# Kernel optimization log

Measured on AMD Instinct MI355X. Metric: run time of the kernel, lower is better.

## Reference

```python
import jax, jax.numpy as jnp
import numpy as np

STATE = 256
HYPER = 256
QHID = 64
NAGENTS = 8


def _lin_init(key, fan_in, fan_out):
    # torch nn.Linear default init: U(-1/sqrt(fan_in), 1/sqrt(fan_in))
    kw, kb = jax.random.split(key)
    bound = 1.0 / np.sqrt(fan_in)
    W = jax.random.uniform(kw, (fan_in, fan_out), jnp.float32, -bound, bound)
    b = jax.random.uniform(kb, (fan_out,), jnp.float32, -bound, bound)
    return W, b


def setup_inputs() -> dict:
    key = jax.random.key(0)
    ks = jax.random.split(key, 8)
    q_value_batch = jax.random.normal(ks[0], (128, 512, NAGENTS, 1), jnp.float32)
    state_batch = jax.random.normal(ks[1], (128, 512, 1, STATE), jnp.float32)
    W1a, b1a = _lin_init(ks[2], STATE, HYPER)
    W1b, b1b = _lin_init(ks[3], HYPER, NAGENTS * QHID)
    W2a, b2a = _lin_init(ks[4], STATE, HYPER)
    W2b, b2b = _lin_init(ks[5], HYPER, QHID)
    Wb1, bb1 = _lin_init(ks[6], STATE, QHID)
    kb2a, kb2b = jax.random.split(ks[7])
    Wb2a, bb2a = _lin_init(kb2a, STATE, QHID)
    Wb2b, bb2b = _lin_init(kb2b, QHID, 1)
    return {
        "q_value_batch": q_value_batch, "state_batch": state_batch,
        "W1a": W1a, "b1a": b1a, "W1b": W1b, "b1b": b1b,
        "W2a": W2a, "b2a": b2a, "W2b": W2b, "b2b": b2b,
        "Wb1": Wb1, "bb1": bb1,
        "Wb2a": Wb2a, "bb2a": bb2a, "Wb2b": Wb2b, "bb2b": bb2b,
    }


def reference(q_value_batch, state_batch,
              W1a, b1a, W1b, b1b,
              W2a, b2a, W2b, b2b,
              Wb1, bb1, Wb2a, bb2a, Wb2b, bb2b):
    B = q_value_batch.shape[0]
    # flatten (num_episode, episode_limit) -> N
    q = q_value_batch.reshape(-1, 1, NAGENTS)          # [N, 1, A]
    s = state_batch.reshape(-1, STATE)                 # [N, S]
    # hypernet w1: S -> H -> A*Q, abs
    w1 = jnp.abs(jax.nn.relu(s @ W1a + b1a) @ W1b + b1b)
    w1 = w1.reshape(-1, NAGENTS, QHID)                 # [N, A, Q]
    b1 = (s @ Wb1 + bb1)[:, None, :]                   # [N, 1, Q]
    hidden = jax.nn.elu(jnp.einsum('nxa,naq->nxq', q, w1) + b1)  # [N, 1, Q]
    # hypernet w2: S -> H -> Q, abs
    w2 = jnp.abs(jax.nn.relu(s @ W2a + b2a) @ W2b + b2b)[:, :, None]  # [N, Q, 1]
    b2 = (jax.nn.relu(s @ Wb2a + bb2a) @ Wb2b + bb2b)[:, :, None]     # [N, 1, 1]
    q_total = jnp.einsum('nxq,nqo->nxo', hidden, w2) + b2             # [N, 1, 1]
    return q_total.reshape(B, -1, 1)
```

## Files before the change

kernel.cpp:

```cpp
#include <hip/hip_runtime.h>

typedef __bf16 bf16_t;
typedef bf16_t bf16x8 __attribute__((ext_vector_type(8)));
typedef bf16_t bf16x4 __attribute__((ext_vector_type(4)));
typedef float f32x4 __attribute__((ext_vector_type(4)));
typedef float fv4 __attribute__((ext_vector_type(4)));

#define MFMA __builtin_amdgcn_mfma_f32_16x16x32_bf16
#define SWZ(row, off) ((off) ^ (((row) & 7) << 4))

#define F_W1A   0
#define F_W2A   65536
#define F_W1B   131072
#define F_W2B   262144
#define F_WB1   278528
#define F_WB2A  294912

__device__ __forceinline__ bf16x8 cvt8(fv4 a, fv4 b) {
  bf16x8 v;
  v[0]=(bf16_t)a[0]; v[1]=(bf16_t)a[1]; v[2]=(bf16_t)a[2]; v[3]=(bf16_t)a[3];
  v[4]=(bf16_t)b[0]; v[5]=(bf16_t)b[1]; v[6]=(bf16_t)b[2]; v[7]=(bf16_t)b[3];
  return v;
}

__global__ __launch_bounds__(256) void cvt_frag(
    const float* __restrict__ W1a, const float* __restrict__ W2a,
    const float* __restrict__ W1b, const float* __restrict__ W2b,
    const float* __restrict__ Wb1, const float* __restrict__ Wb2a,
    bf16_t* __restrict__ ws)
{
  int gid = blockIdx.x * 256 + threadIdx.x;
  const float* src; int start, base, nout;
  if (gid < 8192)       { src = W1a;  start = 0;     base = F_W1A;  nout = 256; }
  else if (gid < 16384) { src = W2a;  start = 8192;  base = F_W2A;  nout = 256; }
  else if (gid < 32768) { src = W1b;  start = 16384; base = F_W1B;  nout = 512; }
  else if (gid < 34816) { src = W2b;  start = 32768; base = F_W2B;  nout = 64;  }
  else if (gid < 36864) { src = Wb1;  start = 34816; base = F_WB1;  nout = 64;  }
  else                  { src = Wb2a; start = 36864; base = F_WB2A; nout = 64;  }
  int local = gid - start;
  int t = local >> 9, kk = (local >> 6) & 7, l = local & 63;
  int n  = t * 16 + (l & 15);
  int k0 = kk * 32 + (l >> 4) * 8;
  bf16x8 v;
  #pragma unroll
  for (int j = 0; j < 8; ++j) v[j] = (bf16_t)src[(k0 + j) * nout + n];
  *(bf16x8*)(ws + base + (size_t)local * 8) = v;
}

#define FRAG(base, tile, kk) \
  (*(const bf16x8*)(ws + (base) + ((size_t)(((tile) * 8 + (kk))) << 9) + lane * 8))

__global__ __launch_bounds__(512) void qmix_f4(
    const float* __restrict__ s, const float* __restrict__ q,
    const bf16_t* __restrict__ ws,
    const float* __restrict__ b1a, const float* __restrict__ b2a,
    const float* __restrict__ b1b, const float* __restrict__ b2b,
    const float* __restrict__ bb1, const float* __restrict__ bb2a,
    const float* __restrict__ Wb2b, const float* __restrict__ bb2b,
    float* __restrict__ out)
{
  __shared__ __align__(16) char sT[64 * 512];
  __shared__ __align__(16) char h1T[64 * 512];
  __shared__ __align__(16) char h2T[64 * 512];
  __shared__ __align__(16) char b1T[64 * 128];
  __shared__ __align__(16) char w2T[64 * 128];
  __shared__ __align__(16) char hidT[2][64 * 256];
  __shared__ float b2part[4][64];

  const int tid = threadIdx.x, wave = tid >> 6, lane = tid & 63;
  const int r16 = lane & 15, g = lane >> 4;
  const int row0 = blockIdx.x * 256;
  const int srow = tid >> 3, sc = tid & 7;

  {
    const fv4* p = (const fv4*)(s + (size_t)(row0 + srow) * 256 + sc * 32);
    #pragma unroll
    for (int j = 0; j < 4; ++j) {
      fv4 a = __builtin_nontemporal_load(p + j * 2);
      fv4 b = __builtin_nontemporal_load(p + j * 2 + 1);
      *(bf16x8*)(&sT[srow * 512 + SWZ(srow, sc * 64 + j * 16)]) = cvt8(a, b);
    }
  }
  __syncthreads();

  const float bb2b0 = bb2b[0];
  const int smBase = (wave < 4) ? (F_WB1 + wave * 4096) : (F_WB2A + (wave - 4) * 4096);

  #pragma unroll 1
  for (int rt = 0; rt < 4; ++rt) {
    const int rowt = row0 + rt * 64;
    {
      f32x4 acc[2][4];
      #pragma unroll
      for (int t = 0; t < 2; ++t)
        #pragma unroll
        for (int h = 0; h < 4; ++h) acc[t][h] = (f32x4)0.f;
      #pragma unroll 2
      for (int kk = 0; kk < 8; ++kk) {
        bf16x8 A0 = FRAG(F_W1A, wave, kk);
        bf16x8 A1 = FRAG(F_W1A, wave + 8, kk);
        #pragma unroll
        for (int h = 0; h < 4; ++h) {
          int rr = h * 16 + r16;
          bf16x8 B = *(const bf16x8*)(&sT[rr * 512 + SWZ(rr, kk * 64 + g * 16)]);
          acc[0][h] = MFMA(A0, B, acc[0][h], 0, 0, 0);
          acc[1][h] = MFMA(A1, B, acc[1][h], 0, 0, 0);
        }
      }
      #pragma unroll
      for (int t8 = 0; t8 < 2; ++t8) {
        float4 bh = *(const float4*)(b1a + (wave + t8 * 8) * 16 + 4 * g);
        #pragma unroll
        for (int h = 0; h < 4; ++h) {
          int rr = h * 16 + r16;
          f32x4 x = acc[t8][h];
          bf16x4 v;
          v[0]=(bf16_t)fmaxf(x[0]+bh.x,0.f); v[1]=(bf16_t)fmaxf(x[1]+bh.y,0.f);
          v[2]=(bf16_t)fmaxf(x[2]+bh.z,0.f); v[3]=(bf16_t)fmaxf(x[3]+bh.w,0.f);
          *(bf16x4*)(&h1T[rr * 512 + SWZ(rr, (wave + t8 * 8) * 32 + 8 * g)]) = v;
        }
      }
    }
    {
      f32x4 acc[2][4];
      #pragma unroll
      for (int t = 0; t < 2; ++t)
        #pragma unroll
        for (int h = 0; h < 4; ++h) acc[t][h] = (f32x4)0.f;
      #pragma unroll 2
      for (int kk = 0; kk < 8; ++kk) {
        bf16x8 A0 = FRAG(F_W2A, wave, kk);
        bf16x8 A1 = FRAG(F_W2A, wave + 8, kk);
        #pragma unroll
        for (int h = 0; h < 4; ++h) {
          int rr = h * 16 + r16;
          bf16x8 B = *(const bf16x8*)(&sT[rr * 512 + SWZ(rr, kk * 64 + g * 16)]);
          acc[0][h] = MFMA(A0, B, acc[0][h], 0, 0, 0);
          acc[1][h] = MFMA(A1, B, acc[1][h], 0, 0, 0);
        }
      }
      #pragma unroll
      for (int t8 = 0; t8 < 2; ++t8) {
        float4 bh = *(const float4*)(b2a + (wave + t8 * 8) * 16 + 4 * g);
        #pragma unroll
        for (int h = 0; h < 4; ++h) {
          int rr = h * 16 + r16;
          f32x4 x = acc[t8][h];
          bf16x4 v;
          v[0]=(bf16_t)fmaxf(x[0]+bh.x,0.f); v[1]=(bf16_t)fmaxf(x[1]+bh.y,0.f);
          v[2]=(bf16_t)fmaxf(x[2]+bh.z,0.f); v[3]=(bf16_t)fmaxf(x[3]+bh.w,0.f);
          *(bf16x4*)(&h2T[rr * 512 + SWZ(rr, (wave + t8 * 8) * 32 + 8 * g)]) = v;
        }
      }
    }
    {
      f32x4 aS[4];
      #pragma unroll
      for (int h = 0; h < 4; ++h) aS[h] = (f32x4)0.f;
      #pragma unroll
      for (int kk = 0; kk < 8; ++kk) {
        bf16x8 A = *(const bf16x8*)(ws + smBase + ((size_t)kk << 9) + lane * 8);
        #pragma unroll
        for (int h = 0; h < 4; ++h) {
          int rr = h * 16 + r16;
          bf16x8 B = *(const bf16x8*)(&sT[rr * 512 + SWZ(rr, kk * 64 + g * 16)]);
          aS[h] = MFMA(A, B, aS[h], 0, 0, 0);
        }
      }
      if (wave < 4) {
        float4 bb = *(const float4*)(bb1 + wave * 16 + 4 * g);
        #pragma unroll
        for (int h = 0; h < 4; ++h) {
          int rr = h * 16 + r16;
          bf16x4 o;
          o[0]=(bf16_t)(aS[h][0]+bb.x); o[1]=(bf16_t)(aS[h][1]+bb.y);
          o[2]=(bf16_t)(aS[h][2]+bb.z); o[3]=(bf16_t)(aS[h][3]+bb.w);
          *(bf16x4*)(&b1T[rr * 128 + wave * 32 + 8 * g]) = o;
        }
      } else {
        float4 ba = *(const float4*)(bb2a + (wave - 4) * 16 + 4 * g);
        float4 wv = *(const float4*)(Wb2b + (wave - 4) * 16 + 4 * g);
        #pragma unroll
        for (int h = 0; h < 4; ++h) {
          int rr = h * 16 + r16;
          f32x4 x = aS[h];
          float part = fmaxf(x[0]+ba.x,0.f)*wv.x + fmaxf(x[1]+ba.y,0.f)*wv.y
                     + fmaxf(x[2]+ba.z,0.f)*wv.z + fmaxf(x[3]+ba.w,0.f)*wv.w;
          part += __shfl_xor(part, 16); part += __shfl_xor(part, 32);
          if (lane < 16) b2part[wave - 4][rr] = part;
        }
      }
    }
    __syncthreads();

    fv4 pf[8];
    if (rt < 3) {
      const fv4* p = (const fv4*)(s + (size_t)(rowt + 64 + srow) * 256 + sc * 32);
      #pragma unroll
      for (int j = 0; j < 8; ++j) pf[j] = __builtin_nontemporal_load(p + j);
    }
    {
      const int tq = wave & 3, hs = wave >> 2;
      f32x4 av[2]; av[0] = (f32x4)0.f; av[1] = (f32x4)0.f;
      #pragma unroll
      for (int kk = 0; kk < 8; ++kk) {
        bf16x8 A = FRAG(F_W2B, tq, kk);
        #pragma unroll
        for (int hh = 0; hh < 2; ++hh) {
          int rr = hs * 32 + hh * 16 + r16;
          bf16x8 B = *(const bf16x8*)(&h2T[rr * 512 + SWZ(rr, kk * 64 + g * 16)]);
          av[hh] = MFMA(A, B, av[hh], 0, 0, 0);
        }
      }
      float4 bv = *(const float4*)(b2b + tq * 16 + 4 * g);
      #pragma unroll
      for (int hh = 0; hh < 2; ++hh) {
        int rr = hs * 32 + hh * 16 + r16;
        bf16x4 o;
        o[0]=(bf16_t)fabsf(av[hh][0]+bv.x); o[1]=(bf16_t)fabsf(av[hh][1]+bv.y);
        o[2]=(bf16_t)fabsf(av[hh][2]+bv.z); o[3]=(bf16_t)fabsf(av[hh][3]+bv.w);
        *(bf16x4*)(&w2T[rr * 128 + tq * 32 + 8 * g]) = o;
      }
    }
    {
      const int tq = wave & 3, ah = wave >> 2;
      #pragma unroll 1
      for (int h = 0; h < 4; ++h) {
        const int rr = h * 16 + r16;
        bf16x8 B[8];
        #pragma unroll
        for (int kk = 0; kk < 8; ++kk)
          B[kk] = *(const bf16x8*)(&h1T[rr * 512 + SWZ(rr, kk * 64 + g * 16)]);
        f32x4 hid = (f32x4)0.f;
        #pragma unroll 2
        for (int aa = 0; aa < 4; ++aa) {
          const int a = ah * 4 + aa;
          f32x4 a2 = (f32x4)0.f;
          #pragma unroll
          for (int kk = 0; kk < 8; ++kk) {
            bf16x8 A = FRAG(F_W1B, a * 4 + tq, kk);
            a2 = MFMA(A, B[kk], a2, 0, 0, 0);
          }
          float qa = q[(size_t)(rowt + rr) * 8 + a];
          float4 bb = *(const float4*)(b1b + a * 64 + tq * 16 + 4 * g);
          hid[0] += qa * fabsf(a2[0] + bb.x);
          hid[1] += qa * fabsf(a2[1] + bb.y);
          hid[2] += qa * fabsf(a2[2] + bb.z);
          hid[3] += qa * fabsf(a2[3] + bb.w);
        }
        *(f32x4*)(&hidT[ah][rr * 256 + SWZ(rr, tq * 64 + g * 16)]) = hid;
      }
    }
    if (rt < 3) {
      #pragma unroll
      for (int j = 0; j < 4; ++j)
        *(bf16x8*)(&sT[srow * 512 + SWZ(srow, sc * 64 + j * 16)]) =
            cvt8(pf[j * 2], pf[j * 2 + 1]);
    }
    __syncthreads();
    {
      const int row = tid >> 3, c = tid & 7;
      f32x4 sA0 = *(const f32x4*)(&hidT[0][row * 256 + SWZ(row, c * 32)]);
      f32x4 sA1 = *(const f32x4*)(&hidT[0][row * 256 + SWZ(row, c * 32 + 16)]);
      f32x4 sB0 = *(const f32x4*)(&hidT[1][row * 256 + SWZ(row, c * 32)]);
      f32x4 sB1 = *(const f32x4*)(&hidT[1][row * 256 + SWZ(row, c * 32 + 16)]);
      bf16x8 b1v = *(const bf16x8*)(&b1T[row * 128 + c * 16]);
      bf16x8 wv  = *(const bf16x8*)(&w2T[row * 128 + c * 16]);
      float d = 0.f;
      #pragma unroll
      for (int e = 0; e < 4; ++e) {
        float h0 = sA0[e] + sB0[e] + (float)b1v[e];
        float h1 = sA1[e] + sB1[e] + (float)b1v[4 + e];
        h0 = h0 > 0.f ? h0 : (__expf(h0) - 1.f);
        h1 = h1 > 0.f ? h1 : (__expf(h1) - 1.f);
        d += h0 * (float)wv[e] + h1 * (float)wv[4 + e];
      }
      d += __shfl_xor(d, 1); d += __shfl_xor(d, 2); d += __shfl_xor(d, 4);
      if (c == 0) {
        float b2v = b2part[0][row] + b2part[1][row] + b2part[2][row]
                  + b2part[3][row] + bb2b0;
        out[rowt + row] = d + b2v;
      }
    }
    __syncthreads();
  }
}

extern "C" void kernel_launch(void* const* d_in, const int* in_sizes, int n_in,
                              void* d_out, int out_size, void* d_ws, size_t ws_size,
                              hipStream_t stream) {
  const float* q    = (const float*)d_in[0];
  const float* s    = (const float*)d_in[1];
  const float* W1a  = (const float*)d_in[2];
  const float* b1a  = (const float*)d_in[3];
  const float* W1b  = (const float*)d_in[4];
  const float* b1b  = (const float*)d_in[5];
  const float* W2a  = (const float*)d_in[6];
  const float* b2a  = (const float*)d_in[7];
  const float* W2b  = (const float*)d_in[8];
  const float* b2b  = (const float*)d_in[9];
  const float* Wb1  = (const float*)d_in[10];
  const float* bb1  = (const float*)d_in[11];
  const float* Wb2a = (const float*)d_in[12];
  const float* bb2a = (const float*)d_in[13];
  const float* Wb2b = (const float*)d_in[14];
  const float* bb2b = (const float*)d_in[15];
  bf16_t* ws = (bf16_t*)d_ws;
  float* out = (float*)d_out;

  int N  = in_sizes[0] / 8;
  int nb = N / 256;

  cvt_frag<<<152, 256, 0, stream>>>(W1a, W2a, W1b, W2b, Wb1, Wb2a, ws);
  qmix_f4<<<nb, 512, 0, stream>>>(s, q, ws, b1a, b2a, b1b, b2b,
                                  bb1, bb2a, Wb2b, bb2b, out);
}
```

Before: 122.9 us.

## Fuse state-layer GEMMs into one pass and reuse W1b fragments across rows

Measured after the change: 152.4 us. 24.0% more time.

```diff
diff --git a/kernel.cpp b/kernel.cpp
--- a/kernel.cpp
+++ b/kernel.cpp
@@ -50,7 +50,7 @@
 #define FRAG(base, tile, kk) \
   (*(const bf16x8*)(ws + (base) + ((size_t)(((tile) * 8 + (kk))) << 9) + lane * 8))
 
-__global__ __launch_bounds__(512) void qmix_f4(
+__global__ __launch_bounds__(512) void qmix_f5(
     const float* __restrict__ s, const float* __restrict__ q,
     const bf16_t* __restrict__ ws,
     const float* __restrict__ b1a, const float* __restrict__ b2a,
@@ -64,7 +64,8 @@
   __shared__ __align__(16) char h2T[64 * 512];
   __shared__ __align__(16) char b1T[64 * 128];
   __shared__ __align__(16) char w2T[64 * 128];
-  __shared__ __align__(16) char hidT[2][64 * 256];
+  __shared__ __align__(16) float hidT[2][64 * 68];
+  __shared__ float qT[512];
   __shared__ float b2part[4][64];
 
   const int tid = threadIdx.x, wave = tid >> 6, lane = tid & 63;
@@ -80,6 +81,7 @@
       fv4 b = __builtin_nontemporal_load(p + j * 2 + 1);
       *(bf16x8*)(&sT[srow * 512 + SWZ(srow, sc * 64 + j * 16)]) = cvt8(a, b);
     }
+    qT[tid] = q[(size_t)row0 * 8 + tid];
   }
   __syncthreads();
 
@@ -90,81 +92,44 @@
   for (int rt = 0; rt < 4; ++rt) {
     const int rowt = row0 + rt * 64;
     {
-      f32x4 acc[2][4];
-      #pragma unroll
-      for (int t = 0; t < 2; ++t)
+      f32x4 acc[5][4];
+      #pragma unroll
+      for (int t = 0; t < 5; ++t)
         #pragma unroll
         for (int h = 0; h < 4; ++h) acc[t][h] = (f32x4)0.f;
       #pragma unroll 2
       for (int kk = 0; kk < 8; ++kk) {
         bf16x8 A0 = FRAG(F_W1A, wave, kk);
         bf16x8 A1 = FRAG(F_W1A, wave + 8, kk);
+        bf16x8 A2 = FRAG(F_W2A, wave, kk);
+        bf16x8 A3 = FRAG(F_W2A, wave + 8, kk);
+        bf16x8 A4 = *(const bf16x8*)(ws + smBase + ((size_t)kk << 9) + lane * 8);
         #pragma unroll
         for (int h = 0; h < 4; ++h) {
           int rr = h * 16 + r16;
           bf16x8 B = *(const bf16x8*)(&sT[rr * 512 + SWZ(rr, kk * 64 + g * 16)]);
           acc[0][h] = MFMA(A0, B, acc[0][h], 0, 0, 0);
           acc[1][h] = MFMA(A1, B, acc[1][h], 0, 0, 0);
+          acc[2][h] = MFMA(A2, B, acc[2][h], 0, 0, 0);
+          acc[3][h] = MFMA(A3, B, acc[3][h], 0, 0, 0);
+          acc[4][h] = MFMA(A4, B, acc[4][h], 0, 0, 0);
         }
       }
       #pragma unroll
       for (int t8 = 0; t8 < 2; ++t8) {
-        float4 bh = *(const float4*)(b1a + (wave + t8 * 8) * 16 + 4 * g);
-        #pragma unroll
-        for (int h = 0; h < 4; ++h) {
-          int rr = h * 16 + r16;
-          f32x4 x = acc[t8][h];
-          bf16x4 v;
-          v[0]=(bf16_t)fmaxf(x[0]+bh.x,0.f); v[1]=(bf16_t)fmaxf(x[1]+bh.y,0.f);
-          v[2]=(bf16_t)fmaxf(x[2]+bh.z,0.f); v[3]=(bf16_t)fmaxf(x[3]+bh.w,0.f);
-          *(bf16x4*)(&h1T[rr * 512 + SWZ(rr, (wave + t8 * 8) * 32 + 8 * g)]) = v;
-        }
-      }
-    }
-    {
-      f32x4 acc[2][4];
-      #pragma unroll
-      for (int t = 0; t < 2; ++t)
-        #pragma unroll
-        for (int h = 0; h < 4; ++h) acc[t][h] = (f32x4)0.f;
-      #pragma unroll 2
-      for (int kk = 0; kk < 8; ++kk) {
-        bf16x8 A0 = FRAG(F_W2A, wave, kk);
-        bf16x8 A1 = FRAG(F_W2A, wave + 8, kk);
-        #pragma unroll
-        for (int h = 0; h < 4; ++h) {
-          int rr = h * 16 + r16;
-          bf16x8 B = *(const bf16x8*)(&sT[rr * 512 + SWZ(rr, kk * 64 + g * 16)]);
-          acc[0][h] = MFMA(A0, B, acc[0][h], 0, 0, 0);
-          acc[1][h] = MFMA(A1, B, acc[1][h], 0, 0, 0);
-        }
-      }
-      #pragma unroll
-      for (int t8 = 0; t8 < 2; ++t8) {
-        float4 bh = *(const float4*)(b2a + (wave + t8 * 8) * 16 + 4 * g);
-        #pragma unroll
-        for (int h = 0; h < 4; ++h) {
-          int rr = h * 16 + r16;
-          f32x4 x = acc[t8][h];
-          bf16x4 v;
-          v[0]=(bf16_t)fmaxf(x[0]+bh.x,0.f); v[1]=(bf16_t)fmaxf(x[1]+bh.y,0.f);
-          v[2]=(bf16_t)fmaxf(x[2]+bh.z,0.f); v[3]=(bf16_t)fmaxf(x[3]+bh.w,0.f);
-          *(bf16x4*)(&h2T[rr * 512 + SWZ(rr, (wave + t8 * 8) * 32 + 8 * g)]) = v;
-        }
-      }
-    }
-    {
-      f32x4 aS[4];
-      #pragma unroll
-      for (int h = 0; h < 4; ++h) aS[h] = (f32x4)0.f;
-      #pragma unroll
-      for (int kk = 0; kk < 8; ++kk) {
-        bf16x8 A = *(const bf16x8*)(ws + smBase + ((size_t)kk << 9) + lane * 8);
-        #pragma unroll
-        for (int h = 0; h < 4; ++h) {
-          int rr = h * 16 + r16;
-          bf16x8 B = *(const bf16x8*)(&sT[rr * 512 + SWZ(rr, kk * 64 + g * 16)]);
-          aS[h] = MFMA(A, B, aS[h], 0, 0, 0);
+        float4 bh1 = *(const float4*)(b1a + (wave + t8 * 8) * 16 + 4 * g);
+        float4 bh2 = *(const float4*)(b2a + (wave + t8 * 8) * 16 + 4 * g);
+        #pragma unroll
+        for (int h = 0; h < 4; ++h) {
+          int rr = h * 16 + r16;
+          f32x4 x1 = acc[t8][h], x2 = acc[2 + t8][h];
+          bf16x4 v1, v2;
+          v1[0]=(bf16_t)fmaxf(x1[0]+bh1.x,0.f); v1[1]=(bf16_t)fmaxf(x1[1]+bh1.y,0.f);
+          v1[2]=(bf16_t)fmaxf(x1[2]+bh1.z,0.f); v1[3]=(bf16_t)fmaxf(x1[3]+bh1.w,0.f);
+          v2[0]=(bf16_t)fmaxf(x2[0]+bh2.x,0.f); v2[1]=(bf16_t)fmaxf(x2[1]+bh2.y,0.f);
+          v2[2]=(bf16_t)fmaxf(x2[2]+bh2.z,0.f); v2[3]=(bf16_t)fmaxf(x2[3]+bh2.w,0.f);
+          *(bf16x4*)(&h1T[rr * 512 + SWZ(rr, (wave + t8 * 8) * 32 + 8 * g)]) = v1;
+          *(bf16x4*)(&h2T[rr * 512 + SWZ(rr, (wave + t8 * 8) * 32 + 8 * g)]) = v2;
         }
       }
       if (wave < 4) {
@@ -173,8 +138,8 @@
         for (int h = 0; h < 4; ++h) {
           int rr = h * 16 + r16;
           bf16x4 o;
-          o[0]=(bf16_t)(aS[h][0]+bb.x); o[1]=(bf16_t)(aS[h][1]+bb.y);
-          o[2]=(bf16_t)(aS[h][2]+bb.z); o[3]=(bf16_t)(aS[h][3]+bb.w);
+          o[0]=(bf16_t)(acc[4][h][0]+bb.x); o[1]=(bf16_t)(acc[4][h][1]+bb.y);
+          o[2]=(bf16_t)(acc[4][h][2]+bb.z); o[3]=(bf16_t)(acc[4][h][3]+bb.w);
           *(bf16x4*)(&b1T[rr * 128 + wave * 32 + 8 * g]) = o;
         }
       } else {
@@ -183,7 +148,7 @@
         #pragma unroll
         for (int h = 0; h < 4; ++h) {
           int rr = h * 16 + r16;
-          f32x4 x = aS[h];
+          f32x4 x = acc[4][h];
           float part = fmaxf(x[0]+ba.x,0.f)*wv.x + fmaxf(x[1]+ba.y,0.f)*wv.y
                      + fmaxf(x[2]+ba.z,0.f)*wv.z + fmaxf(x[3]+ba.w,0.f)*wv.w;
           part += __shfl_xor(part, 16); part += __shfl_xor(part, 32);
@@ -194,10 +159,12 @@
     __syncthreads();
 
     fv4 pf[8];
+    float qn;
     if (rt < 3) {
       const fv4* p = (const fv4*)(s + (size_t)(rowt + 64 + srow) * 256 + sc * 32);
       #pragma unroll
       for (int j = 0; j < 8; ++j) pf[j] = __builtin_nontemporal_load(p + j);
+      qn = q[(size_t)(rowt + 64) * 8 + tid];
     }
     {
       const int tq = wave & 3, hs = wave >> 2;
@@ -224,31 +191,43 @@
     }
     {
       const int tq = wave & 3, ah = wave >> 2;
+      f32x4 hid[4];
+      #pragma unroll
+      for (int h = 0; h < 4; ++h) hid[h] = (f32x4)0.f;
       #pragma unroll 1
-      for (int h = 0; h < 4; ++h) {
-        const int rr = h * 16 + r16;
-        bf16x8 B[8];
-        #pragma unroll
-        for (int kk = 0; kk < 8; ++kk)
-          B[kk] = *(const bf16x8*)(&h1T[rr * 512 + SWZ(rr, kk * 64 + g * 16)]);
-        f32x4 hid = (f32x4)0.f;
-        #pragma unroll 2
-        for (int aa = 0; aa < 4; ++aa) {
-          const int a = ah * 4 + aa;
-          f32x4 a2 = (f32x4)0.f;
+      for (int aa = 0; aa < 4; ++aa) {
+        const int a = ah * 4 + aa;
+        bf16x8 A[8];
+        #pragma unroll
+        for (int kk = 0; kk < 8; ++kk) A[kk] = FRAG(F_W1B, a * 4 + tq, kk);
+        float4 bb = *(const float4*)(b1b + a * 64 + tq * 16 + 4 * g);
+        #pragma unroll
+        for (int hp = 0; hp < 2; ++hp) {
+          const int rr0 = hp * 32 + r16, rr1 = hp * 32 + 16 + r16;
+          f32x4 a20 = (f32x4)0.f, a21 = (f32x4)0.f;
           #pragma unroll
           for (int kk = 0; kk < 8; ++kk) {
-            bf16x8 A = FRAG(F_W1B, a * 4 + tq, kk);
-            a2 = MFMA(A, B[kk], a2, 0, 0, 0);
+            bf16x8 B0 = *(const bf16x8*)(&h1T[rr0 * 512 + SWZ(rr0, kk * 64 + g * 16)]);
+            bf16x8 B1 = *(const bf16x8*)(&h1T[rr1 * 512 + SWZ(rr1, kk * 64 + g * 16)]);
+            a20 = MFMA(A[kk], B0, a20, 0, 0, 0);
+            a21 = MFMA(A[kk], B1, a21, 0, 0, 0);
           }
-          float qa = q[(size_t)(rowt + rr) * 8 + a];
-          float4 bb = *(const float4*)(b1b + a * 64 + tq * 16 + 4 * g);
-          hid[0] += qa * fabsf(a2[0] + bb.x);
-          hid[1] += qa * fabsf(a2[1] + bb.y);
-          hid[2] += qa * fabsf(a2[2] + bb.z);
-          hid[3] += qa * fabsf(a2[3] + bb.w);
-        }
-        *(f32x4*)(&hidT[ah][rr * 256 + SWZ(rr, tq * 64 + g * 16)]) = hid;
+          float qa0 = qT[rr0 * 8 + a];
+          float qa1 = qT[rr1 * 8 + a];
+          hid[hp*2+0][0] += qa0 * fabsf(a20[0] + bb.x);
+          hid[hp*2+0][1] += qa0 * fabsf(a20[1] + bb.y);
+          hid[hp*2+0][2] += qa0 * fabsf(a20[2] + bb.z);
+          hid[hp*2+0][3] += qa0 * fabsf(a20[3] + bb.w);
+          hid[hp*2+1][0] += qa1 * fabsf(a21[0] + bb.x);
+          hid[hp*2+1][1] += qa1 * fabsf(a21[1] + bb.y);
+          hid[hp*2+1][2] += qa1 * fabsf(a21[2] + bb.z);
+          hid[hp*2+1][3] += qa1 * fabsf(a21[3] + bb.w);
+        }
+      }
+      #pragma unroll
+      for (int h = 0; h < 4; ++h) {
+        int rr = h * 16 + r16;
+        *(f32x4*)(&hidT[ah][rr * 68 + tq * 16 + g * 4]) = hid[h];
       }
     }
     if (rt < 3) {
@@ -256,14 +235,15 @@
       for (int j = 0; j < 4; ++j)
         *(bf16x8*)(&sT[srow * 512 + SWZ(srow, sc * 64 + j * 16)]) =
             cvt8(pf[j * 2], pf[j * 2 + 1]);
+      qT[tid] = qn;
     }
     __syncthreads();
     {
       const int row = tid >> 3, c = tid & 7;
-      f32x4 sA0 = *(const f32x4*)(&hidT[0][row * 256 + SWZ(row, c * 32)]);
-      f32x4 sA1 = *(const f32x4*)(&hidT[0][row * 256 + SWZ(row, c * 32 + 16)]);
-      f32x4 sB0 = *(const f32x4*)(&hidT[1][row * 256 + SWZ(row, c * 32)]);
-      f32x4 sB1 = *(const f32x4*)(&hidT[1][row * 256 + SWZ(row, c * 32 + 16)]);
+      f32x4 sA0 = *(const f32x4*)(&hidT[0][row * 68 + c * 8]);
+      f32x4 sA1 = *(const f32x4*)(&hidT[0][row * 68 + c * 8 + 4]);
+      f32x4 sB0 = *(const f32x4*)(&hidT[1][row * 68 + c * 8]);
+      f32x4 sB1 = *(const f32x4*)(&hidT[1][row * 68 + c * 8 + 4]);
       bf16x8 b1v = *(const bf16x8*)(&b1T[row * 128 + c * 16]);
       bf16x8 wv  = *(const bf16x8*)(&w2T[row * 128 + c * 16]);
       float d = 0.f;
@@ -312,6 +292,6 @@
   int nb = N / 256;
 
   cvt_frag<<<152, 256, 0, stream>>>(W1a, W2a, W1b, W2b, Wb1, Wb2a, ws);
-  qmix_f4<<<nb, 512, 0, stream>>>(s, q, ws, b1a, b2a, b1b, b2b,
+  qmix_f5<<<nb, 512, 0, stream>>>(s, q, ws, b1a, b2a, b1b, b2b,
                                   bb1, bb2a, Wb2b, bb2b, out);
 }
```
